# Kernel optimization log

Measured on AMD Instinct MI355X. Metric: run time of the kernel, lower is better.

Reference implementation:

```python
import jax, jax.numpy as jnp
import numpy as np

D_MODEL = 1024
NUM_HEADS = 16
DEPTH = D_MODEL // NUM_HEADS
NEG_INF_SCALE = -1e9


def setup_inputs() -> dict:
    key = jax.random.key(0)
    ks = jax.random.split(key, 12)
    B, S = 2, 2048
    q = jax.random.normal(ks[0], (B, S, D_MODEL), dtype=jnp.float32)
    k = jax.random.normal(ks[1], (B, S, D_MODEL), dtype=jnp.float32)
    v = jax.random.normal(ks[2], (B, S, D_MODEL), dtype=jnp.float32)
    # causal mask: 1 where attention is disallowed (future positions)
    mask = jnp.triu(jnp.ones((S, S), dtype=jnp.float32), k=1)[None, None]
    scale = 1.0 / np.sqrt(D_MODEL)
    Wq = jax.random.normal(ks[3], (D_MODEL, D_MODEL), dtype=jnp.float32) * scale
    bq = jnp.zeros((D_MODEL,), dtype=jnp.float32)
    Wk = jax.random.normal(ks[4], (D_MODEL, D_MODEL), dtype=jnp.float32) * scale
    bk = jnp.zeros((D_MODEL,), dtype=jnp.float32)
    Wv = jax.random.normal(ks[5], (D_MODEL, D_MODEL), dtype=jnp.float32) * scale
    bv = jnp.zeros((D_MODEL,), dtype=jnp.float32)
    Wo = jax.random.normal(ks[6], (D_MODEL, D_MODEL), dtype=jnp.float32) * scale
    bo = jnp.zeros((D_MODEL,), dtype=jnp.float32)
    return {"v": v, "k": k, "q": q, "mask": mask,
            "Wq": Wq, "bq": bq, "Wk": Wk, "bk": bk,
            "Wv": Wv, "bv": bv, "Wo": Wo, "bo": bo}


def _split_heads(x):
    B, S, _ = x.shape
    return x.reshape(B, S, NUM_HEADS, DEPTH).transpose(0, 2, 1, 3)  # [B,H,S,depth]


def reference(v, k, q, mask, Wq, bq, Wk, bk, Wv, bv, Wo, bo):
    B, Sq, _ = q.shape
    qh = _split_heads(q @ Wq + bq)  # [B,H,Sq,depth]
    kh = _split_heads(k @ Wk + bk)  # [B,H,Sk,depth]
    vh = _split_heads(v @ Wv + bv)  # [B,H,Sk,depth]
    logits = jnp.einsum('bhqd,bhkd->bhqk', qh, kh) / jnp.sqrt(
        jnp.asarray(DEPTH, dtype=jnp.float32))
    logits = logits + mask * NEG_INF_SCALE
    attn = jax.nn.softmax(logits, axis=-1)
    out = jnp.einsum('bhqk,bhkd->bhqd', attn, vh)  # [B,H,Sq,depth]
    out = out.transpose(0, 2, 1, 3).reshape(B, Sq, D_MODEL)
    return out @ Wo + bo
```

## Files before the change

kernel.cpp:

```cpp
#include <hip/hip_runtime.h>
#include <stdint.h>

#define D_MODEL 1024
#define NHEADS  16
#define DEPTH   64
#define BATCH   2
#define SEQ     2048
#define M_TOT   (BATCH * SEQ)

#define Q_SCALE 0.18033688011112042f

typedef unsigned short u16;
typedef unsigned int   u32;
typedef __attribute__((ext_vector_type(8))) short bf16x8;
typedef __attribute__((ext_vector_type(4))) float f32x4;

__device__ __forceinline__ float bf2f(unsigned int u) {
    union { unsigned int i; float f; } x;
    x.i = (u & 0xffffu) << 16;
    return x.f;
}
__device__ __forceinline__ u16 f2bf(float f) {
    union { float f; unsigned int i; } x;
    x.f = f;
    unsigned int lsb = (x.i >> 16) & 1u;
    x.i += 0x7fffu + lsb;
    return (u16)(x.i >> 16);
}
__device__ __forceinline__ u32 fbits(float f) {
    union { float f; unsigned int i; } x; x.f = f; return x.i;
}
__device__ __forceinline__ float exp2f_hw(float x) {
    return __builtin_amdgcn_exp2f(x);
}

template <int CTRL>
__device__ __forceinline__ float dppf(float x) {
    int r = __builtin_amdgcn_update_dpp(0, (int)fbits(x), CTRL, 0xF, 0xF, false);
    union { int i; float f; } u; u.i = r; return u.f;
}
__device__ __forceinline__ float redmax16(float x) {
    x = fmaxf(x, dppf<0xB1>(x));
    x = fmaxf(x, dppf<0x4E>(x));
    x = fmaxf(x, dppf<0x124>(x));
    x = fmaxf(x, dppf<0x128>(x));
    return x;
}
__device__ __forceinline__ float redsum16(float x) {
    x += dppf<0xB1>(x);
    x += dppf<0x4E>(x);
    x += dppf<0x124>(x);
    x += dppf<0x128>(x);
    return x;
}

__device__ __forceinline__ void stage16(const u16* g, u16* ldsbase) {
#if __has_builtin(__builtin_amdgcn_global_load_lds)
    __builtin_amdgcn_global_load_lds(
        (const __attribute__((address_space(1))) unsigned int*)g,
        (__attribute__((address_space(3))) unsigned int*)ldsbase, 16, 0, 0);
#else
    int lane = threadIdx.x & 63;
    *(uint4*)(ldsbase + lane * 8) = *(const uint4*)g;
#endif
}

__global__ void sniff_kernel(const u16* __restrict__ q, int* __restrict__ flag) {
    const int t = threadIdx.x;
    int cnt = 0;
    #pragma unroll
    for (int j = 0; j < 4; ++j) {
        unsigned int bits = q[2 * (t + 64 * j)];
        bool susp = ((bits & 0x7fffu) >= 0x4780u);
        cnt += (int)__popcll(__ballot(susp));
    }
    if (t == 0) flag[0] = (cnt >= 32) ? 1 : 0;
}

__global__ __launch_bounds__(256)
void conv_kernel(const void* s0, const void* s1, const void* s2,
                 u16* d0, u16* d1, u16* d2, const int* __restrict__ flag) {
    const int z = blockIdx.z;
    const void* src = (z == 0) ? s0 : (z == 1) ? s1 : s2;
    u16* dst = (z == 0) ? d0 : (z == 1) ? d1 : d2;
    const int f32 = *flag;
    const size_t i = ((size_t)blockIdx.x * 256 + threadIdx.x) * 8;
    if (f32) {
        const float* s = (const float*)src + i;
        float4 a = *(const float4*)s;
        float4 b = *(const float4*)(s + 4);
        u16 t8[8];
        t8[0] = f2bf(a.x); t8[1] = f2bf(a.y); t8[2] = f2bf(a.z); t8[3] = f2bf(a.w);
        t8[4] = f2bf(b.x); t8[5] = f2bf(b.y); t8[6] = f2bf(b.z); t8[7] = f2bf(b.w);
        *(uint4*)(dst + i) = *(uint4*)t8;
    } else {
        *(uint4*)(dst + i) = *(const uint4*)((const u16*)src + i);
    }
}

__global__ __launch_bounds__(256)
void wT_kernel(const void* W0, const void* W1, const void* W2, const void* W3,
               u16* T0, u16* T1, u16* T2, u16* T3, const int* __restrict__ flag) {
    __shared__ u16 t[64][72];
    const int z = blockIdx.z;
    const void* Wv = (z == 0) ? W0 : (z == 1) ? W1 : (z == 2) ? W2 : W3;
    u16* WT = (z == 0) ? T0 : (z == 1) ? T1 : (z == 2) ? T2 : T3;
    const int f32 = *flag;
    const int tid = threadIdx.x;
    const int n0 = blockIdx.x * 64, k0 = blockIdx.y * 64;

    #pragma unroll
    for (int cb = 0; cb < 2; ++cb) {
        int c = tid + cb * 256;
        int kl = c >> 3, nc = (c & 7) * 8;
        size_t off = (size_t)(k0 + kl) * D_MODEL + n0 + nc;
        u16 tmp[8];
        if (f32) {
            const float* W = (const float*)Wv;
            float4 a = *(const float4*)(W + off);
            float4 b = *(const float4*)(W + off + 4);
            tmp[0] = f2bf(a.x); tmp[1] = f2bf(a.y); tmp[2] = f2bf(a.z); tmp[3] = f2bf(a.w);
            tmp[4] = f2bf(b.x); tmp[5] = f2bf(b.y); tmp[6] = f2bf(b.z); tmp[7] = f2bf(b.w);
        } else {
            *(uint4*)tmp = *(const uint4*)((const u16*)Wv + off);
        }
        *(uint4*)&t[kl][nc] = *(uint4*)tmp;
    }
    __syncthreads();
    #pragma unroll
    for (int cb = 0; cb < 2; ++cb) {
        int c = tid + cb * 256;
        int nl = c >> 3, kc = (c & 7) * 8;
        u16 tmp[8];
        #pragma unroll
        for (int i = 0; i < 8; ++i) tmp[i] = t[kc + i][nl];
        *(uint4*)(WT + (size_t)(n0 + nl) * D_MODEL + k0 + kc) = *(uint4*)tmp;
    }
}

struct GemmJob {
    const u16*  A;
    const u16*  BT;
    const void* bias;
    void*       C;
    int cmode;
    float scale;
};

__global__ __launch_bounds__(256)
void gemm6(GemmJob j0, GemmJob j1, GemmJob j2, const int* __restrict__ flag) {
    __shared__ u16 Als[128 * 64];
    __shared__ u16 Bls[128 * 64];

    const u32 lin = blockIdx.x + gridDim.x * (blockIdx.y + gridDim.y * blockIdx.z);
    const u32 xcd = lin & 7, idx = lin >> 3;
    const u32 per = (gridDim.y * gridDim.z) >> 3;
    const u32 mz = xcd * per + (idx >> 3);
    const u32 nb_ = idx & 7;
    const u32 zz = mz / gridDim.y;
    const u32 my = mz % gridDim.y;
    GemmJob jb = (zz == 0) ? j0 : (zz == 1) ? j1 : j2;

    const int f32 = *flag;
    const int tid = threadIdx.x;
    const int w = tid >> 6, lane = tid & 63;
    const int cc = lane & 15, quad = lane >> 4;
    const int wm = w >> 1, wn = w & 1;
    const int m0 = my * 128, n0 = nb_ * 128;

    f32x4 zero4 = {0.f, 0.f, 0.f, 0.f};
    f32x4 acc[4][4];
    #pragma unroll
    for (int i = 0; i < 4; ++i)
        #pragma unroll
        for (int j = 0; j < 4; ++j) acc[i][j] = zero4;

    const int srow_off = lane >> 3;
    const int sg8 = ((lane & 7) ^ ((lane >> 3) & 7)) * 8;

    for (int k0 = 0; k0 < D_MODEL; k0 += 64) {
        __syncthreads();
        #pragma unroll
        for (int i = 0; i < 4; ++i) {
            int c = w * 4 + i;
            int row = c * 8 + srow_off;
            stage16(jb.BT + (size_t)(n0 + row) * D_MODEL + k0 + sg8, &Bls[c * 512]);
            stage16(jb.A  + (size_t)(m0 + row) * D_MODEL + k0 + sg8, &Als[c * 512]);
        }
        __syncthreads();

        const int sw = cc & 7;
        bf16x8 af[4][2], bf[4][2];
        #pragma unroll
        for (int i = 0; i < 4; ++i) {
            const u16* ar = &Als[(wm * 64 + i * 16 + cc) * 64];
            af[i][0] = *(const bf16x8*)(ar + ((quad ^ sw) * 8));
            af[i][1] = *(const bf16x8*)(ar + (((4 + quad) ^ sw) * 8));
        }
        #pragma unroll
        for (int j = 0; j < 4; ++j) {
            const u16* br = &Bls[(wn * 64 + j * 16 + cc) * 64];
            bf[j][0] = *(const bf16x8*)(br + ((quad ^ sw) * 8));
            bf[j][1] = *(const bf16x8*)(br + (((4 + quad) ^ sw) * 8));
        }
        #pragma unroll
        for (int i = 0; i < 4; ++i)
            #pragma unroll
            for (int j = 0; j < 4; ++j) {
                acc[i][j] = __builtin_amdgcn_mfma_f32_16x16x32_bf16(af[i][0], bf[j][0], acc[i][j], 0, 0, 0);
                acc[i][j] = __builtin_amdgcn_mfma_f32_16x16x32_bf16(af[i][1], bf[j][1], acc[i][j], 0, 0, 0);
            }
    }

    #pragma unroll
    for (int j = 0; j < 4; ++j) {
        int col = n0 + wn * 64 + j * 16 + cc;
        float bv = f32 ? ((const float*)jb.bias)[col] : bf2f(((const u16*)jb.bias)[col]);
        #pragma unroll
        for (int i = 0; i < 4; ++i)
            #pragma unroll
            for (int r = 0; r < 4; ++r) {
                int row = m0 + wm * 64 + i * 16 + quad * 4 + r;
                float vo = (acc[i][j][r] + bv) * jb.scale;
                if (jb.cmode == 0) {
                    ((u16*)jb.C)[(size_t)row * D_MODEL + col] = f2bf(vo);
                } else if (jb.cmode == 1) {
                    int bb = row >> 11, tok = row & (SEQ - 1);
                    int hh = col >> 6, dd = col & 63;
                    int tile = tok >> 6, n = tok & 63;
                    int kap = ((n & 15) << 2) + (n >> 4);
                    ((u16*)jb.C)[((size_t)((bb * NHEADS + hh) * DEPTH + dd)) * SEQ
                                 + tile * 64 + kap] = f2bf(vo);
                } else {
                    if (f32) ((float*)jb.C)[(size_t)row * D_MODEL + col] = vo;
                    else     ((u16*)jb.C)[(size_t)row * D_MODEL + col] = f2bf(vo);
                }
            }
    }
}

__global__ __launch_bounds__(256, 3)
void attn3(const u16* __restrict__ Qp, const u16* __restrict__ Kp,
           const u16* __restrict__ VpT, u16* __restrict__ Ao) {
    __shared__ u16 Kls[2][64 * 64];
    __shared__ u16 Vls[2][64 * 64];
    __shared__ u16 Pls[4][32][72];

    const int tid = threadIdx.x;
    const int w = tid >> 6, lane = tid & 63;
    const int cc = lane & 15, quad = lane >> 4;
    const int qt = (int)(gridDim.x - 1 - blockIdx.x);
    const int h = blockIdx.y, b = blockIdx.z;
    const int qbase = qt * 128 + w * 32;

    bf16x8 qf[2][2];
    #pragma unroll
    for (int mi = 0; mi < 2; ++mi) {
        const u16* qr = Qp + (size_t)(b * SEQ + qbase + mi * 16 + cc) * D_MODEL + h * DEPTH;
        qf[mi][0] = *(const bf16x8*)(qr + quad * 8);
        qf[mi][1] = *(const bf16x8*)(qr + 32 + quad * 8);
    }

    const u16* kbase = Kp + (size_t)(b * SEQ) * D_MODEL + h * DEPTH;
    const u16* vbase = VpT + (size_t)((b * NHEADS + h) * DEPTH) * SEQ;

    const int r8 = lane >> 3;
    const int g8 = ((lane & 7) ^ (r8 & 7)) * 8;

    auto stageKV = [&](int buf, int jt) {
        #pragma unroll
        for (int i = 0; i < 2; ++i) {
            int row = w * 16 + i * 8 + r8;
            stage16(kbase + (size_t)(jt * 64 + row) * D_MODEL + g8,
                    &Kls[buf][(w * 16 + i * 8) * 64]);
            stage16(vbase + (size_t)row * SEQ + jt * 64 + g8,
                    &Vls[buf][(w * 16 + i * 8) * 64]);
        }
    };

    f32x4 zero4 = {0.f, 0.f, 0.f, 0.f};
    f32x4 oacc[2][4];
    #pragma unroll
    for (int mi = 0; mi < 2; ++mi)
        #pragma unroll
        for (int db = 0; db < 4; ++db) oacc[mi][db] = zero4;
    float m_run[2][4], l_run[2][4];
    #pragma unroll
    for (int mi = 0; mi < 2; ++mi)
        #pragma unroll
        for (int r = 0; r < 4; ++r) { m_run[mi][r] = -1e30f; l_run[mi][r] = 0.f; }

    const int jtmax = 2 * qt + 1;
    stageKV(0, 0);

    for (int jt = 0; jt <= jtmax; ++jt) {
        const int cur = jt & 1;
        __syncthreads();
        if (jt < jtmax) stageKV(cur ^ 1, jt + 1);

        if (jt * 64 > qbase + 31) continue;

        const int sw = cc & 7;
        bf16x8 kf[4][2];
        #pragma unroll
        for (int nb = 0; nb < 4; ++nb) {
            const u16* kr = &Kls[cur][(nb * 16 + cc) * 64];
            kf[nb][0] = *(const bf16x8*)(kr + ((quad ^ sw) * 8));
            kf[nb][1] = *(const bf16x8*)(kr + (((4 + quad) ^ sw) * 8));
        }
        f32x4 s[2][4];
        #pragma unroll
        for (int mi = 0; mi < 2; ++mi)
            #pragma unroll
            for (int nb = 0; nb < 4; ++nb) {
                s[mi][nb] = __builtin_amdgcn_mfma_f32_16x16x32_bf16(qf[mi][0], kf[nb][0], zero4, 0, 0, 0);
                s[mi][nb] = __builtin_amdgcn_mfma_f32_16x16x32_bf16(qf[mi][1], kf[nb][1], s[mi][nb], 0, 0, 0);
            }
        #pragma unroll
        for (int mi = 0; mi < 2; ++mi) {
            if (jt * 64 + 63 > qbase + mi * 16) {
                #pragma unroll
                for (int nb = 0; nb < 4; ++nb)
                    #pragma unroll
                    for (int r = 0; r < 4; ++r)
                        if (jt * 64 + nb * 16 + cc > qbase + mi * 16 + quad * 4 + r)
                            s[mi][nb][r] = -1e30f;
            }
        }

        float alpha[2][4];
        #pragma unroll
        for (int mi = 0; mi < 2; ++mi) {
            #pragma unroll
            for (int r = 0; r < 4; ++r) {
                float mrow = redmax16(fmaxf(fmaxf(s[mi][0][r], s[mi][1][r]),
                                            fmaxf(s[mi][2][r], s[mi][3][r])));
                float mn = fmaxf(m_run[mi][r], mrow);
                alpha[mi][r] = exp2f_hw(m_run[mi][r] - mn);
                m_run[mi][r] = mn;
            }
            #pragma unroll
            for (int nb = 0; nb < 4; ++nb)
                #pragma unroll
                for (int r = 0; r < 4; ++r)
                    s[mi][nb][r] = exp2f_hw(s[mi][nb][r] - m_run[mi][r]);
            #pragma unroll
            for (int r = 0; r < 4; ++r)
                l_run[mi][r] = l_run[mi][r] * alpha[mi][r]
                             + ((s[mi][0][r] + s[mi][1][r]) + (s[mi][2][r] + s[mi][3][r]));
            #pragma unroll
            for (int db = 0; db < 4; ++db)
                #pragma unroll
                for (int r = 0; r < 4; ++r)
                    oacc[mi][db][r] *= alpha[mi][r];
        }

        #pragma unroll
        for (int mi = 0; mi < 2; ++mi)
            #pragma unroll
            for (int r = 0; r < 4; ++r) {
                u32 p01 = __builtin_amdgcn_perm(fbits(s[mi][1][r]), fbits(s[mi][0][r]), 0x07060302u);
                u32 p23 = __builtin_amdgcn_perm(fbits(s[mi][3][r]), fbits(s[mi][2][r]), 0x07060302u);
                uint2 pk; pk.x = p01; pk.y = p23;
                *(uint2*)&Pls[w][mi * 16 + quad * 4 + r][4 * cc] = pk;
            }
        __asm__ volatile("" ::: "memory");

        bf16x8 pf[2][2];
        #pragma unroll
        for (int mi = 0; mi < 2; ++mi) {
            pf[mi][0] = *(const bf16x8*)&Pls[w][mi * 16 + cc][quad * 8];
            pf[mi][1] = *(const bf16x8*)&Pls[w][mi * 16 + cc][32 + quad * 8];
        }
        #pragma unroll
        for (int db = 0; db < 4; ++db) {
            const u16* vr = &Vls[cur][(db * 16 + cc) * 64];
            bf16x8 v0 = *(const bf16x8*)(vr + ((quad ^ sw) * 8));
            bf16x8 v1 = *(const bf16x8*)(vr + (((4 + quad) ^ sw) * 8));
            #pragma unroll
            for (int mi = 0; mi < 2; ++mi) {
                oacc[mi][db] = __builtin_amdgcn_mfma_f32_16x16x32_bf16(pf[mi][0], v0, oacc[mi][db], 0, 0, 0);
                oacc[mi][db] = __builtin_amdgcn_mfma_f32_16x16x32_bf16(pf[mi][1], v1, oacc[mi][db], 0, 0, 0);
            }
        }
    }

    #pragma unroll
    for (int mi = 0; mi < 2; ++mi) {
        float linv[4];
        #pragma unroll
        for (int r = 0; r < 4; ++r) linv[r] = 1.0f / redsum16(l_run[mi][r]);
        #pragma unroll
        for (int db = 0; db < 4; ++db)
            #pragma unroll
            for (int r = 0; r < 4; ++r) {
                size_t row = (size_t)(b * SEQ + qbase + mi * 16 + quad * 4 + r);
                Ao[row * D_MODEL + h * DEPTH + db * 16 + cc] =
                    f2bf(oacc[mi][db][r] * linv[r]);
            }
    }
}

extern "C" void kernel_launch(void* const* d_in, const int* in_sizes, int n_in,
                              void* d_out, int out_size, void* d_ws, size_t ws_size,
                              hipStream_t stream) {
    const void* v  = d_in[0];
    const void* k  = d_in[1];
    const void* q  = d_in[2];
    const void* Wq = d_in[4];
    const void* bq = d_in[5];
    const void* Wk = d_in[6];
    const void* bk = d_in[7];
    const void* Wv = d_in[8];
    const void* bv = d_in[9];
    const void* Wo = d_in[10];
    const void* bo = d_in[11];

    char* base = (char*)d_ws;
    int* flag = (int*)base;
    const size_t WSZ = (size_t)D_MODEL * D_MODEL;
    const size_t TOK = (size_t)M_TOT * D_MODEL;
    u16* WqT = (u16*)(base + 256);
    u16* WkT = WqT + WSZ;
    u16* WvT = WkT + WSZ;
    u16* WoT = WvT + WSZ;
    u16* Qb  = WoT + WSZ;
    u16* Kb  = Qb + TOK;
    u16* Vb  = Kb + TOK;
    u16* Qp  = Vb + TOK;
    u16* Kp  = Qp + TOK;
    u16* VpT = Kp + TOK;
    u16* Ao  = Qb;

    sniff_kernel<<<1, 64, 0, stream>>>((const u16*)q, flag);

    conv_kernel<<<dim3(2048, 1, 3), 256, 0, stream>>>(q, k, v, Qb, Kb, Vb, flag);
    wT_kernel<<<dim3(16, 16, 4), 256, 0, stream>>>(Wq, Wk, Wv, Wo,
                                                   WqT, WkT, WvT, WoT, flag);

    GemmJob jq = {Qb, WqT, bq, Qp,    0, Q_SCALE};
    GemmJob jk = {Kb, WkT, bk, Kp,    0, 1.0f};
    GemmJob jv = {Vb, WvT, bv, VpT,   1, 1.0f};
    gemm6<<<dim3(8, 32, 3), 256, 0, stream>>>(jq, jk, jv, flag);

    attn3<<<dim3(16, 16, 2), 256, 0, stream>>>(Qp, Kp, VpT, Ao);

    GemmJob jo = {Ao, WoT, bo, d_out, 2, 1.0f};
    gemm6<<<dim3(8, 32, 1), 256, 0, stream>>>(jo, jo, jo, flag);
}
```

Baseline: 299.5 us.

## Replace LDS-staged attention with single-wave blocks loading K/V into registers

Rewrites the attention kernel so that each 64-thread block handles 32 query rows. K and V fragments are loaded directly from global memory into registers, and the next K tile is prefetched one step ahead. This removes the shared-memory double buffering and the per-iteration __syncthreads. Masking now applies only on the final diagonal tile, and the finer grid should balance the causal workload better. In exchange, the four waves that used to share each staged K/V tile now each fetch it separately, which multiplies global/L2 traffic and uses uncoalesced fragment-shaped loads.

```diff
diff --git a/kernel.cpp b/kernel.cpp
--- a/kernel.cpp
+++ b/kernel.cpp
@@ -239,24 +239,22 @@
     }
 }
 
-__global__ __launch_bounds__(256, 3)
-void attn3(const u16* __restrict__ Qp, const u16* __restrict__ Kp,
+__global__ __launch_bounds__(64, 3)
+void attn4(const u16* __restrict__ Qp, const u16* __restrict__ Kp,
            const u16* __restrict__ VpT, u16* __restrict__ Ao) {
-    __shared__ u16 Kls[2][64 * 64];
-    __shared__ u16 Vls[2][64 * 64];
-    __shared__ u16 Pls[4][32][72];
-
-    const int tid = threadIdx.x;
-    const int w = tid >> 6, lane = tid & 63;
+    __shared__ u16 Pls[32][72];
+
+    const int lane = threadIdx.x & 63;
     const int cc = lane & 15, quad = lane >> 4;
-    const int qt = (int)(gridDim.x - 1 - blockIdx.x);
+    const int x = (int)(gridDim.x - 1 - blockIdx.x);
     const int h = blockIdx.y, b = blockIdx.z;
-    const int qbase = qt * 128 + w * 32;
+    const int qb = x * 32;
+    const int jtmax = (qb + 31) >> 6;
 
     bf16x8 qf[2][2];
     #pragma unroll
     for (int mi = 0; mi < 2; ++mi) {
-        const u16* qr = Qp + (size_t)(b * SEQ + qbase + mi * 16 + cc) * D_MODEL + h * DEPTH;
+        const u16* qr = Qp + (size_t)(b * SEQ + qb + mi * 16 + cc) * D_MODEL + h * DEPTH;
         qf[mi][0] = *(const bf16x8*)(qr + quad * 8);
         qf[mi][1] = *(const bf16x8*)(qr + 32 + quad * 8);
     }
@@ -264,20 +262,6 @@
     const u16* kbase = Kp + (size_t)(b * SEQ) * D_MODEL + h * DEPTH;
     const u16* vbase = VpT + (size_t)((b * NHEADS + h) * DEPTH) * SEQ;
 
-    const int r8 = lane >> 3;
-    const int g8 = ((lane & 7) ^ (r8 & 7)) * 8;
-
-    auto stageKV = [&](int buf, int jt) {
-        #pragma unroll
-        for (int i = 0; i < 2; ++i) {
-            int row = w * 16 + i * 8 + r8;
-            stage16(kbase + (size_t)(jt * 64 + row) * D_MODEL + g8,
-                    &Kls[buf][(w * 16 + i * 8) * 64]);
-            stage16(vbase + (size_t)row * SEQ + jt * 64 + g8,
-                    &Vls[buf][(w * 16 + i * 8) * 64]);
-        }
-    };
-
     f32x4 zero4 = {0.f, 0.f, 0.f, 0.f};
     f32x4 oacc[2][4];
     #pragma unroll
@@ -290,24 +274,31 @@
         #pragma unroll
         for (int r = 0; r < 4; ++r) { m_run[mi][r] = -1e30f; l_run[mi][r] = 0.f; }
 
-    const int jtmax = 2 * qt + 1;
-    stageKV(0, 0);
+    bf16x8 kf[4][2];
+    #pragma unroll
+    for (int nb = 0; nb < 4; ++nb) {
+        const u16* kr = kbase + (size_t)(nb * 16 + cc) * D_MODEL;
+        kf[nb][0] = *(const bf16x8*)(kr + quad * 8);
+        kf[nb][1] = *(const bf16x8*)(kr + 32 + quad * 8);
+    }
 
     for (int jt = 0; jt <= jtmax; ++jt) {
-        const int cur = jt & 1;
-        __syncthreads();
-        if (jt < jtmax) stageKV(cur ^ 1, jt + 1);
-
-        if (jt * 64 > qbase + 31) continue;
-
-        const int sw = cc & 7;
-        bf16x8 kf[4][2];
+        bf16x8 vf[4][2];
+        #pragma unroll
+        for (int db = 0; db < 4; ++db) {
+            const u16* vr = vbase + (size_t)(db * 16 + cc) * SEQ + jt * 64;
+            vf[db][0] = *(const bf16x8*)(vr + quad * 8);
+            vf[db][1] = *(const bf16x8*)(vr + 32 + quad * 8);
+        }
+        const int jn = (jt < jtmax) ? jt + 1 : jt;
+        bf16x8 kn[4][2];
         #pragma unroll
         for (int nb = 0; nb < 4; ++nb) {
-            const u16* kr = &Kls[cur][(nb * 16 + cc) * 64];
-            kf[nb][0] = *(const bf16x8*)(kr + ((quad ^ sw) * 8));
-            kf[nb][1] = *(const bf16x8*)(kr + (((4 + quad) ^ sw) * 8));
-        }
+            const u16* kr = kbase + (size_t)(jn * 64 + nb * 16 + cc) * D_MODEL;
+            kn[nb][0] = *(const bf16x8*)(kr + quad * 8);
+            kn[nb][1] = *(const bf16x8*)(kr + 32 + quad * 8);
+        }
+
         f32x4 s[2][4];
         #pragma unroll
         for (int mi = 0; mi < 2; ++mi)
@@ -316,16 +307,15 @@
                 s[mi][nb] = __builtin_amdgcn_mfma_f32_16x16x32_bf16(qf[mi][0], kf[nb][0], zero4, 0, 0, 0);
                 s[mi][nb] = __builtin_amdgcn_mfma_f32_16x16x32_bf16(qf[mi][1], kf[nb][1], s[mi][nb], 0, 0, 0);
             }
-        #pragma unroll
-        for (int mi = 0; mi < 2; ++mi) {
-            if (jt * 64 + 63 > qbase + mi * 16) {
+        if (jt == jtmax) {
+            #pragma unroll
+            for (int mi = 0; mi < 2; ++mi)
                 #pragma unroll
                 for (int nb = 0; nb < 4; ++nb)
                     #pragma unroll
                     for (int r = 0; r < 4; ++r)
-                        if (jt * 64 + nb * 16 + cc > qbase + mi * 16 + quad * 4 + r)
+                        if (jt * 64 + nb * 16 + cc > qb + mi * 16 + quad * 4 + r)
                             s[mi][nb][r] = -1e30f;
-            }
         }
 
         float alpha[2][4];
@@ -362,26 +352,28 @@
                 u32 p01 = __builtin_amdgcn_perm(fbits(s[mi][1][r]), fbits(s[mi][0][r]), 0x07060302u);
                 u32 p23 = __builtin_amdgcn_perm(fbits(s[mi][3][r]), fbits(s[mi][2][r]), 0x07060302u);
                 uint2 pk; pk.x = p01; pk.y = p23;
-                *(uint2*)&Pls[w][mi * 16 + quad * 4 + r][4 * cc] = pk;
+                *(uint2*)&Pls[mi * 16 + quad * 4 + r][4 * cc] = pk;
             }
         __asm__ volatile("" ::: "memory");
 
         bf16x8 pf[2][2];
         #pragma unroll
         for (int mi = 0; mi < 2; ++mi) {
-            pf[mi][0] = *(const bf16x8*)&Pls[w][mi * 16 + cc][quad * 8];
-            pf[mi][1] = *(const bf16x8*)&Pls[w][mi * 16 + cc][32 + quad * 8];
-        }
-        #pragma unroll
-        for (int db = 0; db < 4; ++db) {
-            const u16* vr = &Vls[cur][(db * 16 + cc) * 64];
-            bf16x8 v0 = *(const bf16x8*)(vr + ((quad ^ sw) * 8));
-            bf16x8 v1 = *(const bf16x8*)(vr + (((4 + quad) ^ sw) * 8));
+            pf[mi][0] = *(const bf16x8*)&Pls[mi * 16 + cc][quad * 8];
+            pf[mi][1] = *(const bf16x8*)&Pls[mi * 16 + cc][32 + quad * 8];
+        }
+        #pragma unroll
+        for (int db = 0; db < 4; ++db)
             #pragma unroll
             for (int mi = 0; mi < 2; ++mi) {
-                oacc[mi][db] = __builtin_amdgcn_mfma_f32_16x16x32_bf16(pf[mi][0], v0, oacc[mi][db], 0, 0, 0);
-                oacc[mi][db] = __builtin_amdgcn_mfma_f32_16x16x32_bf16(pf[mi][1], v1, oacc[mi][db], 0, 0, 0);
-            }
+                oacc[mi][db] = __builtin_amdgcn_mfma_f32_16x16x32_bf16(pf[mi][0], vf[db][0], oacc[mi][db], 0, 0, 0);
+                oacc[mi][db] = __builtin_amdgcn_mfma_f32_16x16x32_bf16(pf[mi][1], vf[db][1], oacc[mi][db], 0, 0, 0);
+            }
+
+        #pragma unroll
+        for (int nb = 0; nb < 4; ++nb) {
+            kf[nb][0] = kn[nb][0];
+            kf[nb][1] = kn[nb][1];
         }
     }
 
@@ -394,7 +386,7 @@
         for (int db = 0; db < 4; ++db)
             #pragma unroll
             for (int r = 0; r < 4; ++r) {
-                size_t row = (size_t)(b * SEQ + qbase + mi * 16 + quad * 4 + r);
+                size_t row = (size_t)(b * SEQ + qb + mi * 16 + quad * 4 + r);
                 Ao[row * D_MODEL + h * DEPTH + db * 16 + cc] =
                     f2bf(oacc[mi][db][r] * linv[r]);
             }
@@ -443,7 +435,7 @@
     GemmJob jv = {Vb, WvT, bv, VpT,   1, 1.0f};
     gemm6<<<dim3(8, 32, 3), 256, 0, stream>>>(jq, jk, jv, flag);
 
-    attn3<<<dim3(16, 16, 2), 256, 0, stream>>>(Qp, Kp, VpT, Ao);
+    attn4<<<dim3(64, 16, 2), 64, 0, stream>>>(Qp, Kp, VpT, Ao);
 
     GemmJob jo = {Ao, WoT, bo, d_out, 2, 1.0f};
     gemm6<<<dim3(8, 32, 1), 256, 0, stream>>>(jo, jo, jo, flag);
```

Measured after the change: 372.1 us. 24.2% more time.
